# Kernel tuning notes

Measured on AMD Instinct MI355X. Metric: run time of the kernel, lower is better.

## Reference

```python
import jax, jax.numpy as jnp
import numpy as np

C1 = 0.01 ** 2
C2 = 0.03 ** 2
IN_CH = 3
WIN = 11
LEVELS = 5


def _gauss_kernel(k=WIN, sigma=1.5, c=IN_CH):
    ax = np.arange(k, dtype=np.float32) - (k - 1) / 2.0
    g = np.exp(-(ax ** 2) / (2.0 * sigma ** 2))
    g = g / g.sum()
    w2d = np.outer(g, g).astype(np.float32)  # [k,k]
    return jnp.asarray(np.tile(w2d[None, None], (c, 1, 1, 1)))  # [C,1,k,k]


def _dwconv(x, w):
    # depthwise (grouped) conv, 'same' padding for odd kernel
    pad = (w.shape[-1] - 1) // 2
    return jax.lax.conv_general_dilated(
        x, w, window_strides=(1, 1), padding=[(pad, pad), (pad, pad)],
        feature_group_count=x.shape[1],
        dimension_numbers=("NCHW", "OIHW", "NCHW"))


def _ssim_loss(i1, i2, w):
    m1 = _dwconv(i1, w)
    m2 = _dwconv(i2, w)
    m1sq = m1 * m1
    m2sq = m2 * m2
    m12 = m1 * m2
    s1 = _dwconv(i1 * i1, w) - m1sq
    s2 = _dwconv(i2 * i2, w) - m2sq
    s12 = _dwconv(i1 * i2, w) - m12
    ssim = (2 * m12 + C1) * (2 * s12 + C2) / ((m1sq + m2sq + C1) * (s1 + s2 + C2))
    return 1.0 - ssim.mean()


def _avg_pool2(x):
    B, C, H, W = x.shape
    return x.reshape(B, C, H // 2, 2, W // 2, 2).mean(axis=(3, 5))


def setup_inputs() -> dict:
    key = jax.random.key(0)
    k1, k2 = jax.random.split(key)
    img1 = jax.random.uniform(k1, (16, IN_CH, 512, 512), dtype=jnp.float32)
    img2 = jax.random.uniform(k2, (16, IN_CH, 512, 512), dtype=jnp.float32)
    inp = {"img1": img1, "img2": img2}
    for i in range(LEVELS):
        inp[f"g{i}"] = _gauss_kernel()
    return inp


def reference(img1, img2, g0, g1, g2, g3, g4):
    loss = jnp.asarray(0.0, dtype=img1.dtype)
    for w in (g0, g1, g2, g3, g4):
        loss = loss + _ssim_loss(img1, img2, w)
        img1 = _avg_pool2(img1)
        img2 = _avg_pool2(img2)
    return loss
```

## Files before the change

kernel.cpp:

```cpp
#include <hip/hip_runtime.h>
#include <math.h>

#define WIN 11
#define PAD 5
#define TW 64

typedef float v2f __attribute__((ext_vector_type(2)));

struct GW { float g[WIN]; };

template<bool EMIT>
__device__ __forceinline__ float ssim_wave_tile(
    const float* __restrict__ p1, const float* __restrict__ p2,
    int W, int X0, int Y0, const GW& gw, float2* __restrict__ rb,
    float* __restrict__ o1a, float* __restrict__ o1b, int Wout)
{
    const int TH = 32;
    const int lane = threadIdx.x & 63;
    const int gx = X0 + lane;
    const bool cval = gx < W;
    const int hx   = (lane < 5) ? (X0 - 5 + lane) : (X0 + 59 + lane);
    const bool hval = (lane < 10) && ((unsigned)hx < (unsigned)W);
    const int hpos = (lane < 5) ? lane : (64 + lane);
    const int cpos = 5 + lane;
    const int gxc = cval ? gx : 0;
    const int hxc = hval ? hx : gxc;
    const int wpos = (lane < 10) ? hpos : cpos;

    float vMp[11], vSp[11], vMq[11], vSq[11];
#pragma unroll
    for (int k = 0; k < 11; ++k) { vMp[k] = 0.f; vSp[k] = 0.f; vMq[k] = 0.f; vSq[k] = 0.f; }

    float part = 0.f;
    float pprev = 0.f, qprev = 0.f;

    auto LOAD = [&](int t, float& oa, float& ob, float& oah, float& obh) {
        int y = Y0 - PAD + t;
        bool yin = (unsigned)y < (unsigned)W;
        const float* r1 = p1 + (size_t)(yin ? y : 0) * W;
        const float* r2 = p2 + (size_t)(yin ? y : 0) * W;
        float va = r1[gxc], vb = r2[gxc];
        float wa = r1[hxc], wb = r2[hxc];
        bool cv = yin && cval;
        bool hv = yin && hval;
        oa  = cv ? va : 0.f;
        ob  = cv ? vb : 0.f;
        oah = hv ? wa : 0.f;
        obh = hv ? wb : 0.f;
    };

    float a0, b0, ah0, bh0;
    float a1, b1, ah1, bh1;
    LOAD(0, a0, b0, ah0, bh0);
    LOAD(1, a1, b1, ah1, bh1);

#pragma unroll 1
    for (int blk = 0; blk < 4; ++blk) {
#pragma unroll
        for (int u = 0; u < 11; ++u) {
            const int t = blk * 11 + u;

            float a2, b2, ah2, bh2;
            LOAD(t + 2, a2, b2, ah2, bh2);

            float p = a0 + b0, q = a0 - b0;
            float ph = ah0 + bh0, qh = ah0 - bh0;
            rb[cpos] = make_float2(p, q);
            rb[wpos] = (lane < 10) ? make_float2(ph, qh) : make_float2(p, q);
            __builtin_amdgcn_wave_barrier();

            v2f hM = {0.f, 0.f}, hS = {0.f, 0.f};
#pragma unroll
            for (int j = 0; j < WIN; ++j) {
                float2 v = rb[lane + j];
                v2f vm = { v.x, v.y };
                v2f g2 = { gw.g[j], gw.g[j] };
                hM = __builtin_elementwise_fma(g2, vm, hM);
                hS = __builtin_elementwise_fma(g2, vm * vm, hS);
            }
            __builtin_amdgcn_wave_barrier();
            float hp = hM.x, hq = hM.y, hpp = hS.x, hqq = hS.y;

#pragma unroll
            for (int s = 0; s < 11; ++s) {
                const int widx = 10 - ((s - u + 11) % 11);
                float g = gw.g[widx];
                vMp[s] = fmaf(g, hp,  vMp[s]);
                vSp[s] = fmaf(g, hpp, vSp[s]);
                vMq[s] = fmaf(g, hq,  vMq[s]);
                vSq[s] = fmaf(g, hqq, vSq[s]);
            }

            if (EMIT) {
                if (t >= 6 && t <= TH + 4 && (t & 1) == 0) {
                    float sp_ = p + pprev, sq_ = q + qprev;
                    float sp2 = sp_ + __shfl_down(sp_, 1, 64);
                    float sq2 = sq_ + __shfl_down(sq_, 1, 64);
                    if ((lane & 1) == 0) {
                        float P = sp2 * 0.25f, Q = sq2 * 0.25f;
                        int yo = (t - 6) >> 1;
                        size_t oo = (size_t)((Y0 >> 1) + yo) * Wout + ((X0 >> 1) + (lane >> 1));
                        o1a[oo] = (P + Q) * 0.5f;
                        o1b[oo] = (P - Q) * 0.5f;
                    }
                }
                pprev = p; qprev = q;
            }

            {
                int o = t - 10;
                if ((unsigned)o < (unsigned)TH) {
                    bool yok = (unsigned)(Y0 + o) < (unsigned)W;
                    float Mp = vMp[u], Sp_ = vSp[u], Mq = vMq[u], Sq_ = vSq[u];
                    const float C1v = 1e-4f, C2v = 9e-4f;
                    float A = Mp * Mp, B = Mq * Mq;
                    float ABp = A + B, ABm = A - B;
                    float SSp = Sp_ + Sq_, SSm = Sp_ - Sq_;
                    float n1 = fmaf(0.5f, ABm, C1v);
                    float n2 = fmaf(0.5f, SSm - ABm, C2v);
                    float e1 = fmaf(0.5f, ABp, C1v);
                    float e2 = fmaf(0.5f, SSp - ABp, C2v);
                    float v = (n1 * n2) * __builtin_amdgcn_rcpf(e1 * e2);
                    part += (cval && yok) ? v : 0.f;
                }
                vMp[u] = 0.f; vSp[u] = 0.f; vMq[u] = 0.f; vSq[u] = 0.f;
            }

            a0 = a1; b0 = b1; ah0 = ah1; bh0 = bh1;
            a1 = a2; b1 = b2; ah1 = ah2; bh1 = bh2;

            __builtin_amdgcn_sched_barrier(0);
        }
    }

    return part;
}

__global__ __launch_bounds__(256, 4) void ssim_l0_kernel(
    const float* __restrict__ i1, const float* __restrict__ i2,
    float* __restrict__ a1, float* __restrict__ b1,
    double* __restrict__ acc, GW gw)
{
    __shared__ float2 rbs[4][80];
    const int wid = threadIdx.x >> 6;
    const int w = blockIdx.x * 4 + wid;
    const int img = w >> 7;
    const int tt = w & 127;
    const int tx = tt & 7, ty = tt >> 3;
    const size_t off  = (size_t)img * 512 * 512;
    const size_t ooff = (size_t)img * 256 * 256;

    float part = ssim_wave_tile<true>(i1 + off, i2 + off, 512, tx * 64, ty * 32,
                                      gw, rbs[wid], a1 + ooff, b1 + ooff, 256);
#pragma unroll
    for (int o = 32; o > 0; o >>= 1) part += __shfl_down(part, o, 64);
    if ((threadIdx.x & 63) == 0) atomicAdd(acc, (double)part);
}

__global__ __launch_bounds__(256, 4) void ssim_rest_kernel(
    const float* __restrict__ a1, const float* __restrict__ b1,
    const float* __restrict__ a2, const float* __restrict__ b2,
    const float* __restrict__ a3, const float* __restrict__ b3,
    const float* __restrict__ a4, const float* __restrict__ b4,
    double* __restrict__ acc, GW gw)
{
    __shared__ float2 rbs[4][80];
    const int wid = threadIdx.x >> 6;
    const int w = blockIdx.x * 4 + wid;
    const int img = w / 43;
    const int r = w - img * 43;
    int lvl, tx, ty;
    if (r < 32)      { lvl = 1; tx = r & 3;  ty = r >> 2; }
    else if (r < 40) { lvl = 2; int s = r - 32; tx = s & 1; ty = s >> 1; }
    else if (r < 42) { lvl = 3; tx = 0; ty = r - 40; }
    else             { lvl = 4; tx = 0; ty = 0; }
    const int W = 512 >> lvl;
    const float* p1; const float* p2;
    switch (lvl) {
      case 1:  p1 = a1; p2 = b1; break;
      case 2:  p1 = a2; p2 = b2; break;
      case 3:  p1 = a3; p2 = b3; break;
      default: p1 = a4; p2 = b4; break;
    }
    const size_t off = (size_t)img * W * W;

    float part = ssim_wave_tile<false>(p1 + off, p2 + off, W, tx * 64, ty * 32,
                                       gw, rbs[wid], nullptr, nullptr, 0);
#pragma unroll
    for (int o = 32; o > 0; o >>= 1) part += __shfl_down(part, o, 64);
    if ((threadIdx.x & 63) == 0) atomicAdd(acc + lvl, (double)part);
}

__global__ __launch_bounds__(256) void pool_rest_kernel(
    const float* __restrict__ a1, const float* __restrict__ b1,
    float* __restrict__ a2, float* __restrict__ b2,
    float* __restrict__ a3, float* __restrict__ b3,
    float* __restrict__ a4, float* __restrict__ b4)
{
    __shared__ float l2[32][33];
    __shared__ float l3[16][17];
    const int tid = threadIdx.x;
    const int im = blockIdx.y;
    const int tb = blockIdx.x;
    const int tx = tb & 3, ty = tb >> 2;
    const bool second = im >= 48;
    const int ii = second ? im - 48 : im;
    const float* src = (second ? b1 : a1) + (size_t)ii * 256 * 256;
    float* o2 = (second ? b2 : a2) + (size_t)ii * 128 * 128;
    float* o3 = (second ? b3 : a3) + (size_t)ii * 64 * 64;
    float* o4 = (second ? b4 : a4) + (size_t)ii * 32 * 32;
    const int X0 = tx * 64, Y0 = ty * 64;

#pragma unroll
    for (int k = 0; k < 2; ++k) {
        int idx = tid + k * 256;
        int xp = idx & 15;
        int yo = idx >> 4;
        const float* rp = src + (size_t)(Y0 + 2 * yo) * 256 + (X0 + 4 * xp);
        float4 r0 = *(const float4*)rp;
        float4 r1 = *(const float4*)(rp + 256);
        float v0 = (r0.x + r0.y + r1.x + r1.y) * 0.25f;
        float v1 = (r0.z + r0.w + r1.z + r1.w) * 0.25f;
        l2[yo][2 * xp]     = v0;
        l2[yo][2 * xp + 1] = v1;
        float2* op = (float2*)(o2 + (size_t)((Y0 >> 1) + yo) * 128 + ((X0 >> 1) + 2 * xp));
        *op = make_float2(v0, v1);
    }
    __syncthreads();
    {
        int xo = tid & 15, yo = tid >> 4;
        if (yo < 16) {
            float v = (l2[2*yo][2*xo] + l2[2*yo][2*xo+1] +
                       l2[2*yo+1][2*xo] + l2[2*yo+1][2*xo+1]) * 0.25f;
            l3[yo][xo] = v;
            o3[(size_t)((Y0 >> 2) + yo) * 64 + ((X0 >> 2) + xo)] = v;
        }
    }
    __syncthreads();
    if (tid < 64) {
        int xo = tid & 7, yo = tid >> 3;
        float v = (l3[2*yo][2*xo] + l3[2*yo][2*xo+1] +
                   l3[2*yo+1][2*xo] + l3[2*yo+1][2*xo+1]) * 0.25f;
        o4[(size_t)((Y0 >> 3) + yo) * 32 + ((X0 >> 3) + xo)] = v;
    }
}

__global__ void final_kernel(const double* __restrict__ acc, float* __restrict__ out)
{
    double loss = 0.0;
#pragma unroll
    for (int l = 0; l < 5; ++l) {
        double cnt = 48.0 * (double)(512 >> l) * (double)(512 >> l);
        loss += 1.0 - acc[l] / cnt;
    }
    out[0] = (float)loss;
}

extern "C" void kernel_launch(void* const* d_in, const int* in_sizes, int n_in,
                              void* d_out, int out_size, void* d_ws, size_t ws_size,
                              hipStream_t stream)
{
    const float* img1 = (const float*)d_in[0];
    const float* img2 = (const float*)d_in[1];
    float* out = (float*)d_out;

    GW gw;
    double gs[WIN], sum = 0.0;
    for (int i = 0; i < WIN; ++i) {
        double ax = (double)i - 5.0;
        gs[i] = exp(-(ax * ax) / 4.5);
        sum += gs[i];
    }
    for (int i = 0; i < WIN; ++i) gw.g[i] = (float)(gs[i] / sum);

    double* acc = (double*)d_ws;
    float* base = (float*)((char*)d_ws + 64);
    const size_t n1 = 48ull * 256 * 256;
    const size_t n2 = 48ull * 128 * 128;
    const size_t n3 = 48ull * 64 * 64;
    const size_t n4 = 48ull * 32 * 32;
    float* a1 = base;      float* b1 = a1 + n1;
    float* a2 = b1 + n1;   float* b2 = a2 + n2;
    float* a3 = b2 + n2;   float* b3 = a3 + n3;
    float* a4 = b3 + n3;   float* b4 = a4 + n4;

    hipMemsetAsync(acc, 0, 5 * sizeof(double), stream);

    hipLaunchKernelGGL(ssim_l0_kernel, dim3(1536), dim3(256), 0, stream,
                       img1, img2, a1, b1, acc, gw);

    hipLaunchKernelGGL(pool_rest_kernel, dim3(16, 96), dim3(256), 0, stream,
                       a1, b1, a2, b2, a3, b3, a4, b4);

    hipLaunchKernelGGL(ssim_rest_kernel, dim3(516), dim3(256), 0, stream,
                       a1, b1, a2, b2, a3, b3, a4, b4, acc, gw);

    hipLaunchKernelGGL(final_kernel, dim3(1), dim3(1), 0, stream, acc, out);
}
```

Before: 263.1 us.

## Fuse pyramid pooling into level-0 SSIM kernel and fold final reduction

Computes pyramid levels 2-4 inside the level-0 SSIM kernel using cross-lane shuffles and carried row registers, removing the separate pool kernel and its re-read of the level-1 buffers. The final loss computation moves into the last block of the rest kernel, detected with an atomic done counter, which removes another launch. In exchange, the level-0 kernel takes extra registers and branches, and the last-block pattern relies on correct fences.

```diff
diff --git a/kernel.cpp b/kernel.cpp
--- a/kernel.cpp
+++ b/kernel.cpp
@@ -3,7 +3,6 @@
 
 #define WIN 11
 #define PAD 5
-#define TW 64
 
 typedef float v2f __attribute__((ext_vector_type(2)));
 
@@ -13,7 +12,10 @@
 __device__ __forceinline__ float ssim_wave_tile(
     const float* __restrict__ p1, const float* __restrict__ p2,
     int W, int X0, int Y0, const GW& gw, float2* __restrict__ rb,
-    float* __restrict__ o1a, float* __restrict__ o1b, int Wout)
+    float* __restrict__ o1a, float* __restrict__ o1b,
+    float* __restrict__ o2a, float* __restrict__ o2b,
+    float* __restrict__ o3a, float* __restrict__ o3b,
+    float* __restrict__ o4a, float* __restrict__ o4b)
 {
     const int TH = 32;
     const int lane = threadIdx.x & 63;
@@ -33,6 +35,7 @@
 
     float part = 0.f;
     float pprev = 0.f, qprev = 0.f;
+    float pv1P = 0.f, pv1Q = 0.f, pv2P = 0.f, pv2Q = 0.f, pv3P = 0.f, pv3Q = 0.f;
 
     auto LOAD = [&](int t, float& oa, float& ob, float& oah, float& obh) {
         int y = Y0 - PAD + t;
@@ -96,13 +99,46 @@
                     float sp_ = p + pprev, sq_ = q + qprev;
                     float sp2 = sp_ + __shfl_down(sp_, 1, 64);
                     float sq2 = sq_ + __shfl_down(sq_, 1, 64);
+                    float P = sp2 * 0.25f, Q = sq2 * 0.25f;
+                    int yo = (t - 6) >> 1;
                     if ((lane & 1) == 0) {
-                        float P = sp2 * 0.25f, Q = sq2 * 0.25f;
-                        int yo = (t - 6) >> 1;
-                        size_t oo = (size_t)((Y0 >> 1) + yo) * Wout + ((X0 >> 1) + (lane >> 1));
+                        size_t oo = (size_t)((Y0 >> 1) + yo) * 256 + ((X0 >> 1) + (lane >> 1));
                         o1a[oo] = (P + Q) * 0.5f;
                         o1b[oo] = (P - Q) * 0.5f;
                     }
+                    if (yo & 1) {
+                        float p2s = P + pv1P, q2s = Q + pv1Q;
+                        float P2 = (p2s + __shfl_down(p2s, 2, 64)) * 0.25f;
+                        float Q2 = (q2s + __shfl_down(q2s, 2, 64)) * 0.25f;
+                        int l2r = yo >> 1;
+                        if ((lane & 3) == 0) {
+                            size_t oo = (size_t)((Y0 >> 2) + l2r) * 128 + ((X0 >> 2) + (lane >> 2));
+                            o2a[oo] = (P2 + Q2) * 0.5f;
+                            o2b[oo] = (P2 - Q2) * 0.5f;
+                        }
+                        if (l2r & 1) {
+                            float p3s = P2 + pv2P, q3s = Q2 + pv2Q;
+                            float P3 = (p3s + __shfl_down(p3s, 4, 64)) * 0.25f;
+                            float Q3 = (q3s + __shfl_down(q3s, 4, 64)) * 0.25f;
+                            int l3r = l2r >> 1;
+                            if ((lane & 7) == 0) {
+                                size_t oo = (size_t)((Y0 >> 3) + l3r) * 64 + ((X0 >> 3) + (lane >> 3));
+                                o3a[oo] = (P3 + Q3) * 0.5f;
+                                o3b[oo] = (P3 - Q3) * 0.5f;
+                            }
+                            if (l3r & 1) {
+                                float p4s = P3 + pv3P, q4s = Q3 + pv3Q;
+                                float P4 = (p4s + __shfl_down(p4s, 8, 64)) * 0.25f;
+                                float Q4 = (q4s + __shfl_down(q4s, 8, 64)) * 0.25f;
+                                int l4r = l3r >> 1;
+                                if ((lane & 15) == 0) {
+                                    size_t oo = (size_t)((Y0 >> 4) + l4r) * 32 + ((X0 >> 4) + (lane >> 4));
+                                    o4a[oo] = (P4 + Q4) * 0.5f;
+                                    o4b[oo] = (P4 - Q4) * 0.5f;
+                                }
+                            } else { pv3P = P3; pv3Q = Q3; }
+                        } else { pv2P = P2; pv2Q = Q2; }
+                    } else { pv1P = P; pv1Q = Q; }
                 }
                 pprev = p; qprev = q;
             }
@@ -139,6 +175,9 @@
 __global__ __launch_bounds__(256, 4) void ssim_l0_kernel(
     const float* __restrict__ i1, const float* __restrict__ i2,
     float* __restrict__ a1, float* __restrict__ b1,
+    float* __restrict__ a2, float* __restrict__ b2,
+    float* __restrict__ a3, float* __restrict__ b3,
+    float* __restrict__ a4, float* __restrict__ b4,
     double* __restrict__ acc, GW gw)
 {
     __shared__ float2 rbs[4][80];
@@ -148,10 +187,13 @@
     const int tt = w & 127;
     const int tx = tt & 7, ty = tt >> 3;
     const size_t off  = (size_t)img * 512 * 512;
-    const size_t ooff = (size_t)img * 256 * 256;
-
-    float part = ssim_wave_tile<true>(i1 + off, i2 + off, 512, tx * 64, ty * 32,
-                                      gw, rbs[wid], a1 + ooff, b1 + ooff, 256);
+
+    float part = ssim_wave_tile<true>(
+        i1 + off, i2 + off, 512, tx * 64, ty * 32, gw, rbs[wid],
+        a1 + (size_t)img * 256 * 256, b1 + (size_t)img * 256 * 256,
+        a2 + (size_t)img * 128 * 128, b2 + (size_t)img * 128 * 128,
+        a3 + (size_t)img * 64 * 64,   b3 + (size_t)img * 64 * 64,
+        a4 + (size_t)img * 32 * 32,   b4 + (size_t)img * 32 * 32);
 #pragma unroll
     for (int o = 32; o > 0; o >>= 1) part += __shfl_down(part, o, 64);
     if ((threadIdx.x & 63) == 0) atomicAdd(acc, (double)part);
@@ -162,7 +204,8 @@
     const float* __restrict__ a2, const float* __restrict__ b2,
     const float* __restrict__ a3, const float* __restrict__ b3,
     const float* __restrict__ a4, const float* __restrict__ b4,
-    double* __restrict__ acc, GW gw)
+    double* __restrict__ acc, unsigned int* __restrict__ done,
+    float* __restrict__ out, GW gw)
 {
     __shared__ float2 rbs[4][80];
     const int wid = threadIdx.x >> 6;
@@ -185,75 +228,28 @@
     const size_t off = (size_t)img * W * W;
 
     float part = ssim_wave_tile<false>(p1 + off, p2 + off, W, tx * 64, ty * 32,
-                                       gw, rbs[wid], nullptr, nullptr, 0);
+                                       gw, rbs[wid], nullptr, nullptr,
+                                       nullptr, nullptr, nullptr, nullptr,
+                                       nullptr, nullptr);
 #pragma unroll
     for (int o = 32; o > 0; o >>= 1) part += __shfl_down(part, o, 64);
     if ((threadIdx.x & 63) == 0) atomicAdd(acc + lvl, (double)part);
-}
-
-__global__ __launch_bounds__(256) void pool_rest_kernel(
-    const float* __restrict__ a1, const float* __restrict__ b1,
-    float* __restrict__ a2, float* __restrict__ b2,
-    float* __restrict__ a3, float* __restrict__ b3,
-    float* __restrict__ a4, float* __restrict__ b4)
-{
-    __shared__ float l2[32][33];
-    __shared__ float l3[16][17];
-    const int tid = threadIdx.x;
-    const int im = blockIdx.y;
-    const int tb = blockIdx.x;
-    const int tx = tb & 3, ty = tb >> 2;
-    const bool second = im >= 48;
-    const int ii = second ? im - 48 : im;
-    const float* src = (second ? b1 : a1) + (size_t)ii * 256 * 256;
-    float* o2 = (second ? b2 : a2) + (size_t)ii * 128 * 128;
-    float* o3 = (second ? b3 : a3) + (size_t)ii * 64 * 64;
-    float* o4 = (second ? b4 : a4) + (size_t)ii * 32 * 32;
-    const int X0 = tx * 64, Y0 = ty * 64;
-
-#pragma unroll
-    for (int k = 0; k < 2; ++k) {
-        int idx = tid + k * 256;
-        int xp = idx & 15;
-        int yo = idx >> 4;
-        const float* rp = src + (size_t)(Y0 + 2 * yo) * 256 + (X0 + 4 * xp);
-        float4 r0 = *(const float4*)rp;
-        float4 r1 = *(const float4*)(rp + 256);
-        float v0 = (r0.x + r0.y + r1.x + r1.y) * 0.25f;
-        float v1 = (r0.z + r0.w + r1.z + r1.w) * 0.25f;
-        l2[yo][2 * xp]     = v0;
-        l2[yo][2 * xp + 1] = v1;
-        float2* op = (float2*)(o2 + (size_t)((Y0 >> 1) + yo) * 128 + ((X0 >> 1) + 2 * xp));
-        *op = make_float2(v0, v1);
-    }
+
     __syncthreads();
-    {
-        int xo = tid & 15, yo = tid >> 4;
-        if (yo < 16) {
-            float v = (l2[2*yo][2*xo] + l2[2*yo][2*xo+1] +
-                       l2[2*yo+1][2*xo] + l2[2*yo+1][2*xo+1]) * 0.25f;
-            l3[yo][xo] = v;
-            o3[(size_t)((Y0 >> 2) + yo) * 64 + ((X0 >> 2) + xo)] = v;
+    if (threadIdx.x == 0) {
+        __threadfence();
+        unsigned int prev = atomicAdd(done, 1u);
+        if (prev == gridDim.x - 1) {
+            __threadfence();
+            double loss = 0.0;
+#pragma unroll
+            for (int l = 0; l < 5; ++l) {
+                double cnt = 48.0 * (double)(512 >> l) * (double)(512 >> l);
+                loss += 1.0 - acc[l] / cnt;
+            }
+            out[0] = (float)loss;
         }
     }
-    __syncthreads();
-    if (tid < 64) {
-        int xo = tid & 7, yo = tid >> 3;
-        float v = (l3[2*yo][2*xo] + l3[2*yo][2*xo+1] +
-                   l3[2*yo+1][2*xo] + l3[2*yo+1][2*xo+1]) * 0.25f;
-        o4[(size_t)((Y0 >> 3) + yo) * 32 + ((X0 >> 3) + xo)] = v;
-    }
-}
-
-__global__ void final_kernel(const double* __restrict__ acc, float* __restrict__ out)
-{
-    double loss = 0.0;
-#pragma unroll
-    for (int l = 0; l < 5; ++l) {
-        double cnt = 48.0 * (double)(512 >> l) * (double)(512 >> l);
-        loss += 1.0 - acc[l] / cnt;
-    }
-    out[0] = (float)loss;
 }
 
 extern "C" void kernel_launch(void* const* d_in, const int* in_sizes, int n_in,
@@ -274,6 +270,7 @@
     for (int i = 0; i < WIN; ++i) gw.g[i] = (float)(gs[i] / sum);
 
     double* acc = (double*)d_ws;
+    unsigned int* done = (unsigned int*)((char*)d_ws + 40);
     float* base = (float*)((char*)d_ws + 64);
     const size_t n1 = 48ull * 256 * 256;
     const size_t n2 = 48ull * 128 * 128;
@@ -284,16 +281,11 @@
     float* a3 = b2 + n2;   float* b3 = a3 + n3;
     float* a4 = b3 + n3;   float* b4 = a4 + n4;
 
-    hipMemsetAsync(acc, 0, 5 * sizeof(double), stream);
+    hipMemsetAsync(d_ws, 0, 64, stream);
 
     hipLaunchKernelGGL(ssim_l0_kernel, dim3(1536), dim3(256), 0, stream,
-                       img1, img2, a1, b1, acc, gw);
-
-    hipLaunchKernelGGL(pool_rest_kernel, dim3(16, 96), dim3(256), 0, stream,
-                       a1, b1, a2, b2, a3, b3, a4, b4);
+                       img1, img2, a1, b1, a2, b2, a3, b3, a4, b4, acc, gw);
 
     hipLaunchKernelGGL(ssim_rest_kernel, dim3(516), dim3(256), 0, stream,
-                       a1, b1, a2, b2, a3, b3, a4, b4, acc, gw);
-
-    hipLaunchKernelGGL(final_kernel, dim3(1), dim3(1), 0, stream, acc, out);
-}
+                       a1, b1, a2, b2, a3, b3, a4, b4, acc, done, out, gw);
+}
```

Measured after the change: 266.3 us. About the same (+1.2%).
